# Kernel optimization log

Hardware: AMD Instinct MI355X
Metric: run time of the kernel (lower is better)

Reference implementation:

```python
import jax, jax.numpy as jnp
import numpy as np

B, L, S, D_MODEL, H = 4, 2048, 2048, 512, 8
E = D_MODEL // H  # head dim = 64


def setup_inputs() -> dict:
    key = jax.random.key(0)
    ks = jax.random.split(key, 11)
    s = 1.0 / np.sqrt(D_MODEL)
    return {
        "queries": jax.random.normal(ks[0], (B, L, D_MODEL), jnp.float32),
        "keys": jax.random.normal(ks[1], (B, S, D_MODEL), jnp.float32),
        "values": jax.random.normal(ks[2], (B, S, D_MODEL), jnp.float32),
        "Wq": jax.random.normal(ks[3], (D_MODEL, D_MODEL), jnp.float32) * s,
        "bq": jnp.zeros((D_MODEL,), jnp.float32),
        "Wk": jax.random.normal(ks[4], (D_MODEL, D_MODEL), jnp.float32) * s,
        "bk": jnp.zeros((D_MODEL,), jnp.float32),
        "Wv": jax.random.normal(ks[5], (D_MODEL, D_MODEL), jnp.float32) * s,
        "bv": jnp.zeros((D_MODEL,), jnp.float32),
        "Wo": jax.random.normal(ks[6], (D_MODEL, D_MODEL), jnp.float32) * s,
        "bo": jnp.zeros((D_MODEL,), jnp.float32),
    }


def reference(queries, keys, values, Wq, bq, Wk, bk, Wv, bv, Wo, bo):
    # QKV projections, then split heads: [B, T, H, E]
    q = (queries @ Wq + bq).reshape(B, L, H, E)
    k = (keys @ Wk + bk).reshape(B, S, H, E)
    v = (values @ Wv + bv).reshape(B, S, H, E)
    scale = 1.0 / np.sqrt(E)
    # Naive full attention: materialized [B, H, L, S] scores (as in original)
    scores = jnp.einsum('blhe,bshe->bhls', q, k)
    A = jax.nn.softmax(scale * scores, axis=-1)  # dropout = identity at eval
    out = jnp.einsum('bhls,bshd->blhd', A, v).reshape(B, L, H * E)
    return out @ Wo + bo
```

## Files before the change

kernel.cpp:

```cpp
#include <hip/hip_runtime.h>
#include <hip/hip_bf16.h>


typedef __attribute__((ext_vector_type(8))) short bf8_t;
typedef __attribute__((ext_vector_type(4))) float f4_t;
typedef __attribute__((ext_vector_type(16))) float f16_t;
typedef __attribute__((ext_vector_type(4))) unsigned int u32x4;

#define D_MODEL 512
#define HEADS 8
#define EDIM 64
#define LSEQ 2048
#define NBATCH 4
#define MTOT (NBATCH * LSEQ)

static __device__ __forceinline__ unsigned short f2bf(float f) {
  union { float f; unsigned int u; } x;
  x.f = f;
  unsigned int u = x.u;
  u += 0x7FFFu + ((u >> 16) & 1u);
  return (unsigned short)(u >> 16);
}

static __device__ __forceinline__ unsigned int pack2bf(float a, float b) {
  union { __hip_bfloat162 h; unsigned int u; } c;
  c.h.x = __float2bfloat16(a);
  c.h.y = __float2bfloat16(b);
  return c.u;
}

__global__ void wt_cvt_all(const float* __restrict__ Wq, const float* __restrict__ Wk,
                           const float* __restrict__ Wv, const float* __restrict__ Wo,
                           unsigned short* __restrict__ Wqt, unsigned short* __restrict__ Wkt,
                           unsigned short* __restrict__ Wvt, unsigned short* __restrict__ Wot) {
  __shared__ float tile[64][65];
  const int which = blockIdx.z;
  const float* W = (which == 0) ? Wq : (which == 1) ? Wk : (which == 2) ? Wv : Wo;
  unsigned short* Wt = (which == 0) ? Wqt : (which == 1) ? Wkt : (which == 2) ? Wvt : Wot;
  const int k0 = blockIdx.x * 64, n0 = blockIdx.y * 64;
  const int tx = threadIdx.x & 63;
  const int ty = threadIdx.x >> 6;
#pragma unroll
  for (int i = 0; i < 64; i += 4)
    tile[i + ty][tx] = W[(size_t)(k0 + i + ty) * D_MODEL + n0 + tx];
  __syncthreads();
#pragma unroll
  for (int i = 0; i < 64; i += 4)
    Wt[(size_t)(n0 + i + ty) * D_MODEL + k0 + tx] = f2bf(tile[tx][i + ty]);
}

template <bool AF32>
__device__ __forceinline__ void gemm_core(const void* __restrict__ Av,
                                          const unsigned short* __restrict__ Bt,
                                          void* __restrict__ lAv, unsigned short* __restrict__ lB,
                                          f4_t (&acc)[2][4], int m0, int n0) {
  const int t = threadIdx.x;
  const int lane = t & 63;
  const int w = t >> 6;
  const int wr = w >> 1, wc = w & 1;
  const int r = lane & 15, g = lane >> 4;

  for (int k0 = 0; k0 < D_MODEL; k0 += 32) {
    if constexpr (AF32) {
      const float* A = (const float*)Av;
#pragma unroll
      for (int ii = 0; ii < 2; ++ii) {
        int c = t + ii * 256;
        int row = c >> 3, col = c & 7;
        int colp = col ^ (row & 7);
        const char* ga = (const char*)(A + (size_t)(m0 + row) * D_MODEL + k0 + colp * 4);
        __builtin_amdgcn_global_load_lds((const __attribute__((address_space(1))) void*)ga,
                                         (__attribute__((address_space(3))) void*)((char*)lAv + c * 16),
                                         16, 0, 0);
      }
    } else {
      const unsigned short* A = (const unsigned short*)Av;
      int rowA = t >> 2, cbA = (t & 3) * 16;
      const char* ga = (const char*)(A + (size_t)(m0 + rowA) * D_MODEL + k0) + cbA;
      __builtin_amdgcn_global_load_lds((const __attribute__((address_space(1))) void*)ga,
                                       (__attribute__((address_space(3))) void*)((char*)lAv + t * 16),
                                       16, 0, 0);
    }
#pragma unroll
    for (int ii = 0; ii < 2; ++ii) {
      int c = t + ii * 256;
      int rowB = c >> 2, cbB = (c & 3) * 16;
      const char* gb = (const char*)(Bt + (size_t)(n0 + rowB) * D_MODEL + k0) + cbB;
      __builtin_amdgcn_global_load_lds((const __attribute__((address_space(1))) void*)gb,
                                       (__attribute__((address_space(3))) void*)((char*)lB + c * 16),
                                       16, 0, 0);
    }
    __syncthreads();

    bf8_t af[2], bfv[4];
    if constexpr (AF32) {
      const float* lA = (const float*)lAv;
#pragma unroll
      for (int mi = 0; mi < 2; ++mi) {
        const int row = wr * 32 + mi * 16 + r;
        const f4_t lo = *(const f4_t*)(lA + row * 32 + (((2 * g + 0) ^ (row & 7)) << 2));
        const f4_t hi4 = *(const f4_t*)(lA + row * 32 + (((2 * g + 1) ^ (row & 7)) << 2));
        union { unsigned int u[4]; bf8_t b; } pb;
        pb.u[0] = pack2bf(lo[0], lo[1]);
        pb.u[1] = pack2bf(lo[2], lo[3]);
        pb.u[2] = pack2bf(hi4[0], hi4[1]);
        pb.u[3] = pack2bf(hi4[2], hi4[3]);
        af[mi] = pb.b;
      }
    } else {
      const unsigned short* lA = (const unsigned short*)lAv;
#pragma unroll
      for (int mi = 0; mi < 2; ++mi)
        af[mi] = *(const bf8_t*)(lA + (wr * 32 + mi * 16 + r) * 32 + g * 8);
    }
#pragma unroll
    for (int ni = 0; ni < 4; ++ni)
      bfv[ni] = *(const bf8_t*)(lB + (wc * 64 + ni * 16 + r) * 32 + g * 8);
#pragma unroll
    for (int mi = 0; mi < 2; ++mi)
#pragma unroll
      for (int ni = 0; ni < 4; ++ni)
        acc[mi][ni] = __builtin_amdgcn_mfma_f32_16x16x32_bf16(af[mi], bfv[ni], acc[mi][ni], 0, 0, 0);
    __syncthreads();
  }
}

#define QSCALE 0.18033688011112042f
__global__ __launch_bounds__(256, 4) void qkv_gemm(
    const float* __restrict__ Xq, const float* __restrict__ Xk, const float* __restrict__ Xv,
    const unsigned short* __restrict__ Wqt, const unsigned short* __restrict__ Wkt,
    const unsigned short* __restrict__ Wvt,
    const float* __restrict__ bq, const float* __restrict__ bk, const float* __restrict__ bv,
    unsigned short* __restrict__ Qh, unsigned short* __restrict__ Kh,
    unsigned short* __restrict__ Vt) {
  __shared__ alignas(16) float lA[64 * 32];
  __shared__ alignas(16) unsigned short lB[128 * 32];
  const int z = blockIdx.z;
  const float* A           = (z == 0) ? Xq : (z == 1) ? Xk : Xv;
  const unsigned short* Bt = (z == 0) ? Wqt : (z == 1) ? Wkt : Wvt;
  const float* bias        = (z == 0) ? bq : (z == 1) ? bk : bv;
  const int n0 = blockIdx.x * 128, m0 = blockIdx.y * 64;

  f4_t acc[2][4] = {};
  gemm_core<true>(A, Bt, lA, lB, acc, m0, n0);

  const int lane = threadIdx.x & 63;
  const int w = threadIdx.x >> 6;
  const int wr = w >> 1, wc = w & 1;
  const int r = lane & 15, g = lane >> 4;
#pragma unroll
  for (int mi = 0; mi < 2; ++mi)
#pragma unroll
    for (int ni = 0; ni < 4; ++ni) {
      const int coln = n0 + wc * 64 + ni * 16 + r;
      const float bv_ = bias[coln];
      const int h = coln >> 6, e = coln & 63;
#pragma unroll
      for (int j = 0; j < 4; ++j) {
        const int rowm = m0 + wr * 32 + mi * 16 + g * 4 + j;
        const int b = rowm >> 11, li = rowm & 2047;
        float v = acc[mi][ni][j] + bv_;
        if (z == 0) {
          v *= QSCALE;
          Qh[(((size_t)(b * HEADS + h) * LSEQ + li) << 6) + e] = f2bf(v);
        } else if (z == 1) {
          Kh[(((size_t)(b * HEADS + h) * LSEQ + li) << 6) + e] = f2bf(v);
        } else {
          Vt[(((size_t)(b * HEADS + h) * EDIM + e) << 11) + li] = f2bf(v);
        }
      }
    }
}

__global__ __launch_bounds__(256, 4) void o_gemm(const unsigned short* __restrict__ A,
                                                 const unsigned short* __restrict__ Bt,
                                                 const float* __restrict__ bias,
                                                 float* __restrict__ Cout) {
  __shared__ alignas(16) unsigned short lA[64 * 32];
  __shared__ alignas(16) unsigned short lB[128 * 32];
  const int n0 = blockIdx.x * 128, m0 = blockIdx.y * 64;
  f4_t acc[2][4] = {};
  gemm_core<false>(A, Bt, lA, lB, acc, m0, n0);

  const int lane = threadIdx.x & 63;
  const int w = threadIdx.x >> 6;
  const int wr = w >> 1, wc = w & 1;
  const int r = lane & 15, g = lane >> 4;
#pragma unroll
  for (int mi = 0; mi < 2; ++mi)
#pragma unroll
    for (int ni = 0; ni < 4; ++ni) {
      const int coln = n0 + wc * 64 + ni * 16 + r;
      const float bv_ = bias[coln];
#pragma unroll
      for (int j = 0; j < 4; ++j) {
        const int rowm = m0 + wr * 32 + mi * 16 + g * 4 + j;
        Cout[(size_t)rowm * D_MODEL + coln] = acc[mi][ni][j] + bv_;
      }
    }
}

#define XSTR 68

__device__ __forceinline__ void stage_tile(const unsigned short* __restrict__ Kbase,
                                           const unsigned short* __restrict__ Vbase,
                                           unsigned short* ldsK, unsigned short* ldsV,
                                           int s0, int tg) {
#pragma unroll
  for (int ii = 0; ii < 2; ++ii) {
    int c = tg + ii * 256;
    int row = c >> 3, col = c & 7;
    int colp = col ^ (row & 7);
    const char* gk = (const char*)(Kbase + (size_t)(s0 + row) * EDIM + colp * 8);
    __builtin_amdgcn_global_load_lds((const __attribute__((address_space(1))) void*)gk,
                                     (__attribute__((address_space(3))) void*)((char*)ldsK + c * 16),
                                     16, 0, 0);
    const char* gv = (const char*)(Vbase + (size_t)row * LSEQ + s0 + colp * 8);
    __builtin_amdgcn_global_load_lds((const __attribute__((address_space(1))) void*)gv,
                                     (__attribute__((address_space(3))) void*)((char*)ldsV + c * 16),
                                     16, 0, 0);
  }
}

__global__ __launch_bounds__(512, 4) void flash_attn(const unsigned short* __restrict__ Qh,
                                                     const unsigned short* __restrict__ Kh,
                                                     const unsigned short* __restrict__ Vt,
                                                     unsigned short* __restrict__ Ao) {
  __shared__ alignas(16) unsigned short stg[2][2][2][64 * 64];

  const int t = threadIdx.x;
  const int lane = t & 63;
  const int w = t >> 6;
  const int wg = w >> 2;
  const int wq = w & 3;
  const int tg = t & 255;
  const int qn = lane & 31;
  const int hi = lane >> 5;
  const int bh = blockIdx.y;
  const int q0 = blockIdx.x * 128 + wq * 32;
  const int sbase = wg * (LSEQ / 2);

  bf8_t qf[4];
#pragma unroll
  for (int kst = 0; kst < 4; ++kst)
    qf[kst] = *(const bf8_t*)(Qh + ((size_t)bh * LSEQ + q0 + qn) * EDIM + kst * 16 + hi * 8);

  float l0 = 0.f, l1 = 0.f;
  f16_t oacc[2];
#pragma unroll
  for (int eh = 0; eh < 2; ++eh)
#pragma unroll
    for (int r = 0; r < 16; ++r) oacc[eh][r] = 0.f;

  const unsigned short* Kbase = Kh + (size_t)bh * LSEQ * EDIM;
  const unsigned short* Vbase = Vt + (size_t)bh * EDIM * LSEQ;

  stage_tile(Kbase, Vbase, stg[wg][0][0], stg[wg][0][1], sbase, tg);
  __syncthreads();

  int cur = 0;
  const int NT = LSEQ / 2 / 64;
  for (int kt = 0; kt < NT; ++kt) {
    if (kt + 1 < NT)
      stage_tile(Kbase, Vbase, stg[wg][cur ^ 1][0], stg[wg][cur ^ 1][1],
                 sbase + (kt + 1) * 64, tg);

    const unsigned short* lsK = stg[wg][cur][0];
    const unsigned short* lsV = stg[wg][cur][1];

    bf8_t kf[2][4];
#pragma unroll
    for (int sh = 0; sh < 2; ++sh)
#pragma unroll
      for (int kst = 0; kst < 4; ++kst) {
        const int row = 32 * sh + qn;
        const int ch = (2 * kst + hi) ^ (row & 7);
        kf[sh][kst] = *(const bf8_t*)(&lsK[row * 64 + ch * 8]);
      }
    f16_t sacc[2];
#pragma unroll
    for (int sh = 0; sh < 2; ++sh)
#pragma unroll
      for (int r = 0; r < 16; ++r) sacc[sh][r] = 0.f;
    __builtin_amdgcn_s_setprio(1);
#pragma unroll
    for (int sh = 0; sh < 2; ++sh)
#pragma unroll
      for (int kst = 0; kst < 4; ++kst)
        sacc[sh] = __builtin_amdgcn_mfma_f32_32x32x16_bf16(kf[sh][kst], qf[kst], sacc[sh], 0, 0, 0);
    __builtin_amdgcn_s_setprio(0);

    unsigned int pk[16];
#pragma unroll
    for (int sh = 0; sh < 2; ++sh)
#pragma unroll
      for (int i = 0; i < 8; ++i) {
        const float a = __builtin_amdgcn_exp2f(sacc[sh][2 * i]);
        const float b = __builtin_amdgcn_exp2f(sacc[sh][2 * i + 1]);
        if (sh == 0) l0 += a + b; else l1 += a + b;
        pk[sh * 8 + i] = pack2bf(a, b);
      }

    unsigned int sw[16];
#pragma unroll
    for (int i = 0; i < 16; ++i) sw[i] = __shfl_xor(pk[i], 32);

    bf8_t pvb[4];
#pragma unroll
    for (int t2 = 0; t2 < 4; ++t2) {
      union { u32x4 u; bf8_t b; } pb;
      pb.u[0] = hi ? sw[4 * t2 + 2] : pk[4 * t2 + 0];
      pb.u[1] = hi ? sw[4 * t2 + 3] : pk[4 * t2 + 1];
      pb.u[2] = hi ? pk[4 * t2 + 2] : sw[4 * t2 + 0];
      pb.u[3] = hi ? pk[4 * t2 + 3] : sw[4 * t2 + 1];
      pvb[t2] = pb.b;
    }

    __builtin_amdgcn_s_setprio(1);
#pragma unroll
    for (int eh = 0; eh < 2; ++eh)
#pragma unroll
      for (int t2 = 0; t2 < 4; ++t2) {
        const int row = 32 * eh + qn;
        const int ch = (2 * t2 + hi) ^ (row & 7);
        const bf8_t vf = *(const bf8_t*)(&lsV[row * 64 + ch * 8]);
        oacc[eh] = __builtin_amdgcn_mfma_f32_32x32x16_bf16(vf, pvb[t2], oacc[eh], 0, 0, 0);
      }
    __builtin_amdgcn_s_setprio(0);

    __syncthreads();
    cur ^= 1;
  }

  const float l_lane = l0 + l1;
  const float l_own = l_lane + __shfl_xor(l_lane, 32);
  float* xO = (float*)&stg[0][0][0][0];
  float* xL = xO + 128 * XSTR;

  if (wg == 1) {
#pragma unroll
    for (int eh = 0; eh < 2; ++eh)
#pragma unroll
      for (int k = 0; k < 4; ++k) {
        float4 v4;
        v4.x = oacc[eh][4 * k + 0]; v4.y = oacc[eh][4 * k + 1];
        v4.z = oacc[eh][4 * k + 2]; v4.w = oacc[eh][4 * k + 3];
        *(float4*)(xO + (wq * 32 + qn) * XSTR + 32 * eh + 8 * k + 4 * hi) = v4;
      }
    if (hi == 0) xL[wq * 32 + qn] = l_own;
  }
  __syncthreads();

  if (wg == 0) {
    const float inv = 1.f / (l_own + xL[wq * 32 + qn]);
    const int b = bh >> 3, h = bh & 7;
#pragma unroll
    for (int eh = 0; eh < 2; ++eh)
#pragma unroll
      for (int k = 0; k < 4; ++k) {
        const float4 v4 = *(const float4*)(xO + (wq * 32 + qn) * XSTR + 32 * eh + 8 * k + 4 * hi);
        ushort4 ov;
        ov.x = f2bf((oacc[eh][4 * k + 0] + v4.x) * inv);
        ov.y = f2bf((oacc[eh][4 * k + 1] + v4.y) * inv);
        ov.z = f2bf((oacc[eh][4 * k + 2] + v4.z) * inv);
        ov.w = f2bf((oacc[eh][4 * k + 3] + v4.w) * inv);
        const int e = 32 * eh + 8 * k + 4 * hi;
        *(ushort4*)(Ao + ((size_t)(b * LSEQ + q0 + qn)) * D_MODEL + h * EDIM + e) = ov;
      }
  }
}

extern "C" void kernel_launch(void* const* d_in, const int* in_sizes, int n_in,
                              void* d_out, int out_size, void* d_ws, size_t ws_size,
                              hipStream_t stream) {
  const float* queries = (const float*)d_in[0];
  const float* keys    = (const float*)d_in[1];
  const float* values  = (const float*)d_in[2];
  const float* Wq = (const float*)d_in[3];
  const float* bq = (const float*)d_in[4];
  const float* Wk = (const float*)d_in[5];
  const float* bk = (const float*)d_in[6];
  const float* Wv = (const float*)d_in[7];
  const float* bv = (const float*)d_in[8];
  const float* Wo = (const float*)d_in[9];
  const float* bo = (const float*)d_in[10];

  char* ws = (char*)d_ws;
  const size_t XSZ = (size_t)MTOT * D_MODEL * 2;
  unsigned short* Qh  = (unsigned short*)(ws + 3 * XSZ);
  unsigned short* Kh  = (unsigned short*)(ws + 4 * XSZ);
  unsigned short* Vt  = (unsigned short*)(ws + 5 * XSZ);
  unsigned short* Ao  = (unsigned short*)(ws + 6 * XSZ);
  unsigned short* Wqt = (unsigned short*)(ws + 7 * XSZ);
  unsigned short* Wkt = Wqt + 512 * 512;
  unsigned short* Wvt = Wkt + 512 * 512;
  unsigned short* Wot = Wvt + 512 * 512;

  wt_cvt_all<<<dim3(8, 8, 4), 256, 0, stream>>>(Wq, Wk, Wv, Wo, Wqt, Wkt, Wvt, Wot);

  qkv_gemm<<<dim3(D_MODEL / 128, MTOT / 64, 3), 256, 0, stream>>>(
      queries, keys, values, Wqt, Wkt, Wvt, bq, bk, bv, Qh, Kh, Vt);

  flash_attn<<<dim3(LSEQ / 128, NBATCH * HEADS), 512, 0, stream>>>(Qh, Kh, Vt, Ao);

  o_gemm<<<dim3(D_MODEL / 128, MTOT / 64), 256, 0, stream>>>(Ao, Wot, bo, (float*)d_out);
}
```

Before: 115.5 us.

## Double-buffer GEMM LDS staging and drop setprio in attention loop

The shared GEMM core for the QKV and output projections now uses two LDS buffers, issuing the next K-slice's global-to-LDS loads before computing on the current one. This is meant to hide load latency and removes one barrier per iteration. In exchange it doubles the GEMM kernels' LDS use, which may lower occupancy. The attention loop also drops its s_setprio calls and merges the two row-sum accumulators into one, which changes scheduling and adds a small serial dependency on the sum.

```diff
diff --git a/kernel.cpp b/kernel.cpp
--- a/kernel.cpp
+++ b/kernel.cpp
@@ -28,6 +28,10 @@
   c.h.y = __float2bfloat16(b);
   return c.u;
 }
+
+#define GLOAD_LDS(gptr, lptr)                                                        \
+  __builtin_amdgcn_global_load_lds((const __attribute__((address_space(1))) void*)(gptr), \
+                                   (__attribute__((address_space(3))) void*)(lptr), 16, 0, 0)
 
 __global__ void wt_cvt_all(const float* __restrict__ Wq, const float* __restrict__ Wk,
                            const float* __restrict__ Wv, const float* __restrict__ Wo,
@@ -49,52 +53,68 @@
     Wt[(size_t)(n0 + i + ty) * D_MODEL + k0 + tx] = f2bf(tile[tx][i + ty]);
 }
 
+__device__ __forceinline__ void stage_a_f32(const float* __restrict__ A, float* lA,
+                                            int m0, int k0) {
+  const int t = threadIdx.x;
+#pragma unroll
+  for (int ii = 0; ii < 2; ++ii) {
+    int c = t + ii * 256;
+    int row = c >> 3, col = c & 7;
+    int colp = col ^ (row & 7);
+    GLOAD_LDS((const char*)(A + (size_t)(m0 + row) * D_MODEL + k0 + colp * 4),
+              (char*)lA + c * 16);
+  }
+}
+__device__ __forceinline__ void stage_a_bf16(const unsigned short* __restrict__ A,
+                                             unsigned short* lA, int m0, int k0) {
+  const int t = threadIdx.x;
+  int rowA = t >> 2, cbA = (t & 3) * 16;
+  GLOAD_LDS((const char*)(A + (size_t)(m0 + rowA) * D_MODEL + k0) + cbA, (char*)lA + t * 16);
+}
+__device__ __forceinline__ void stage_b(const unsigned short* __restrict__ Bt,
+                                        unsigned short* lB, int n0, int k0) {
+  const int t = threadIdx.x;
+#pragma unroll
+  for (int ii = 0; ii < 2; ++ii) {
+    int c = t + ii * 256;
+    int rowB = c >> 2, cbB = (c & 3) * 16;
+    GLOAD_LDS((const char*)(Bt + (size_t)(n0 + rowB) * D_MODEL + k0) + cbB, (char*)lB + c * 16);
+  }
+}
+
 template <bool AF32>
 __device__ __forceinline__ void gemm_core(const void* __restrict__ Av,
                                           const unsigned short* __restrict__ Bt,
-                                          void* __restrict__ lAv, unsigned short* __restrict__ lB,
+                                          void* __restrict__ lAv,
+                                          unsigned short* __restrict__ lBv,
                                           f4_t (&acc)[2][4], int m0, int n0) {
   const int t = threadIdx.x;
   const int lane = t & 63;
   const int w = t >> 6;
   const int wr = w >> 1, wc = w & 1;
   const int r = lane & 15, g = lane >> 4;
-
-  for (int k0 = 0; k0 < D_MODEL; k0 += 32) {
-    if constexpr (AF32) {
-      const float* A = (const float*)Av;
-#pragma unroll
-      for (int ii = 0; ii < 2; ++ii) {
-        int c = t + ii * 256;
-        int row = c >> 3, col = c & 7;
-        int colp = col ^ (row & 7);
-        const char* ga = (const char*)(A + (size_t)(m0 + row) * D_MODEL + k0 + colp * 4);
-        __builtin_amdgcn_global_load_lds((const __attribute__((address_space(1))) void*)ga,
-                                         (__attribute__((address_space(3))) void*)((char*)lAv + c * 16),
-                                         16, 0, 0);
-      }
-    } else {
-      const unsigned short* A = (const unsigned short*)Av;
-      int rowA = t >> 2, cbA = (t & 3) * 16;
-      const char* ga = (const char*)(A + (size_t)(m0 + rowA) * D_MODEL + k0) + cbA;
-      __builtin_amdgcn_global_load_lds((const __attribute__((address_space(1))) void*)ga,
-                                       (__attribute__((address_space(3))) void*)((char*)lAv + t * 16),
-                                       16, 0, 0);
+  const int ASZ = 64 * 32;
+
+  if constexpr (AF32) stage_a_f32((const float*)Av, (float*)lAv, m0, 0);
+  else                stage_a_bf16((const unsigned short*)Av, (unsigned short*)lAv, m0, 0);
+  stage_b(Bt, lBv, n0, 0);
+  __syncthreads();
+
+  int cur = 0;
+  const int NK = D_MODEL / 32;
+  for (int ks = 0; ks < NK; ++ks) {
+    if (ks + 1 < NK) {
+      const int kn = (ks + 1) * 32;
+      if constexpr (AF32)
+        stage_a_f32((const float*)Av, (float*)lAv + (cur ^ 1) * ASZ, m0, kn);
+      else
+        stage_a_bf16((const unsigned short*)Av, (unsigned short*)lAv + (cur ^ 1) * ASZ, m0, kn);
+      stage_b(Bt, lBv + (cur ^ 1) * 128 * 32, n0, kn);
     }
-#pragma unroll
-    for (int ii = 0; ii < 2; ++ii) {
-      int c = t + ii * 256;
-      int rowB = c >> 2, cbB = (c & 3) * 16;
-      const char* gb = (const char*)(Bt + (size_t)(n0 + rowB) * D_MODEL + k0) + cbB;
-      __builtin_amdgcn_global_load_lds((const __attribute__((address_space(1))) void*)gb,
-                                       (__attribute__((address_space(3))) void*)((char*)lB + c * 16),
-                                       16, 0, 0);
-    }
-    __syncthreads();
 
     bf8_t af[2], bfv[4];
     if constexpr (AF32) {
-      const float* lA = (const float*)lAv;
+      const float* lA = (const float*)lAv + cur * ASZ;
 #pragma unroll
       for (int mi = 0; mi < 2; ++mi) {
         const int row = wr * 32 + mi * 16 + r;
@@ -108,11 +128,12 @@
         af[mi] = pb.b;
       }
     } else {
-      const unsigned short* lA = (const unsigned short*)lAv;
+      const unsigned short* lA = (const unsigned short*)lAv + cur * ASZ;
 #pragma unroll
       for (int mi = 0; mi < 2; ++mi)
         af[mi] = *(const bf8_t*)(lA + (wr * 32 + mi * 16 + r) * 32 + g * 8);
     }
+    const unsigned short* lB = lBv + cur * 128 * 32;
 #pragma unroll
     for (int ni = 0; ni < 4; ++ni)
       bfv[ni] = *(const bf8_t*)(lB + (wc * 64 + ni * 16 + r) * 32 + g * 8);
@@ -122,6 +143,7 @@
       for (int ni = 0; ni < 4; ++ni)
         acc[mi][ni] = __builtin_amdgcn_mfma_f32_16x16x32_bf16(af[mi], bfv[ni], acc[mi][ni], 0, 0, 0);
     __syncthreads();
+    cur ^= 1;
   }
 }
 
@@ -133,8 +155,8 @@
     const float* __restrict__ bq, const float* __restrict__ bk, const float* __restrict__ bv,
     unsigned short* __restrict__ Qh, unsigned short* __restrict__ Kh,
     unsigned short* __restrict__ Vt) {
-  __shared__ alignas(16) float lA[64 * 32];
-  __shared__ alignas(16) unsigned short lB[128 * 32];
+  __shared__ alignas(16) float lA[2][64 * 32];
+  __shared__ alignas(16) unsigned short lB[2][128 * 32];
   const int z = blockIdx.z;
   const float* A           = (z == 0) ? Xq : (z == 1) ? Xk : Xv;
   const unsigned short* Bt = (z == 0) ? Wqt : (z == 1) ? Wkt : Wvt;
@@ -142,7 +164,7 @@
   const int n0 = blockIdx.x * 128, m0 = blockIdx.y * 64;
 
   f4_t acc[2][4] = {};
-  gemm_core<true>(A, Bt, lA, lB, acc, m0, n0);
+  gemm_core<true>(A, Bt, &lA[0][0], &lB[0][0], acc, m0, n0);
 
   const int lane = threadIdx.x & 63;
   const int w = threadIdx.x >> 6;
@@ -176,11 +198,11 @@
                                                  const unsigned short* __restrict__ Bt,
                                                  const float* __restrict__ bias,
                                                  float* __restrict__ Cout) {
-  __shared__ alignas(16) unsigned short lA[64 * 32];
-  __shared__ alignas(16) unsigned short lB[128 * 32];
+  __shared__ alignas(16) unsigned short lA[2][64 * 32];
+  __shared__ alignas(16) unsigned short lB[2][128 * 32];
   const int n0 = blockIdx.x * 128, m0 = blockIdx.y * 64;
   f4_t acc[2][4] = {};
-  gemm_core<false>(A, Bt, lA, lB, acc, m0, n0);
+  gemm_core<false>(A, Bt, &lA[0][0], &lB[0][0], acc, m0, n0);
 
   const int lane = threadIdx.x & 63;
   const int w = threadIdx.x >> 6;
@@ -211,14 +233,10 @@
     int c = tg + ii * 256;
     int row = c >> 3, col = c & 7;
     int colp = col ^ (row & 7);
-    const char* gk = (const char*)(Kbase + (size_t)(s0 + row) * EDIM + colp * 8);
-    __builtin_amdgcn_global_load_lds((const __attribute__((address_space(1))) void*)gk,
-                                     (__attribute__((address_space(3))) void*)((char*)ldsK + c * 16),
-                                     16, 0, 0);
-    const char* gv = (const char*)(Vbase + (size_t)row * LSEQ + s0 + colp * 8);
-    __builtin_amdgcn_global_load_lds((const __attribute__((address_space(1))) void*)gv,
-                                     (__attribute__((address_space(3))) void*)((char*)ldsV + c * 16),
-                                     16, 0, 0);
+    GLOAD_LDS((const char*)(Kbase + (size_t)(s0 + row) * EDIM + colp * 8),
+              (char*)ldsK + c * 16);
+    GLOAD_LDS((const char*)(Vbase + (size_t)row * LSEQ + s0 + colp * 8),
+              (char*)ldsV + c * 16);
   }
 }
 
@@ -245,7 +263,7 @@
   for (int kst = 0; kst < 4; ++kst)
     qf[kst] = *(const bf8_t*)(Qh + ((size_t)bh * LSEQ + q0 + qn) * EDIM + kst * 16 + hi * 8);
 
-  float l0 = 0.f, l1 = 0.f;
+  float l_lane = 0.f;
   f16_t oacc[2];
 #pragma unroll
   for (int eh = 0; eh < 2; ++eh)
@@ -282,13 +300,11 @@
     for (int sh = 0; sh < 2; ++sh)
 #pragma unroll
       for (int r = 0; r < 16; ++r) sacc[sh][r] = 0.f;
-    __builtin_amdgcn_s_setprio(1);
 #pragma unroll
     for (int sh = 0; sh < 2; ++sh)
 #pragma unroll
       for (int kst = 0; kst < 4; ++kst)
         sacc[sh] = __builtin_amdgcn_mfma_f32_32x32x16_bf16(kf[sh][kst], qf[kst], sacc[sh], 0, 0, 0);
-    __builtin_amdgcn_s_setprio(0);
 
     unsigned int pk[16];
 #pragma unroll
@@ -297,7 +313,7 @@
       for (int i = 0; i < 8; ++i) {
         const float a = __builtin_amdgcn_exp2f(sacc[sh][2 * i]);
         const float b = __builtin_amdgcn_exp2f(sacc[sh][2 * i + 1]);
-        if (sh == 0) l0 += a + b; else l1 += a + b;
+        l_lane += a + b;
         pk[sh * 8 + i] = pack2bf(a, b);
       }
 
@@ -316,7 +332,6 @@
       pvb[t2] = pb.b;
     }
 
-    __builtin_amdgcn_s_setprio(1);
 #pragma unroll
     for (int eh = 0; eh < 2; ++eh)
 #pragma unroll
@@ -326,13 +341,11 @@
         const bf8_t vf = *(const bf8_t*)(&lsV[row * 64 + ch * 8]);
         oacc[eh] = __builtin_amdgcn_mfma_f32_32x32x16_bf16(vf, pvb[t2], oacc[eh], 0, 0, 0);
       }
-    __builtin_amdgcn_s_setprio(0);
 
     __syncthreads();
     cur ^= 1;
   }
 
-  const float l_lane = l0 + l1;
   const float l_own = l_lane + __shfl_xor(l_lane, 32);
   float* xO = (float*)&stg[0][0][0][0];
   float* xL = xO + 128 * XSTR;
```

New measurement: 114.2 us. No clear change (-1.1%).
